# Kernel tuning notes

Measured on AMD Instinct MI355X. Metric: run time of the kernel, lower is better.

Reference implementation:

```python
import jax, jax.numpy as jnp
import numpy as np

N_NODES = 50000
N_EDGES = 800000
IN_FEAT = 256
OUT_FEAT = 256
NUM_RELS = 64
NUM_BASES = 8


def setup_inputs() -> dict:
    key = jax.random.key(0)
    ks = jax.random.split(key, 9)
    x = jax.random.normal(ks[0], (N_NODES, IN_FEAT), dtype=jnp.float32)
    src = jax.random.randint(ks[1], (N_EDGES,), 0, N_NODES, dtype=jnp.int32)
    dst = jax.random.randint(ks[2], (N_EDGES,), 0, N_NODES, dtype=jnp.int32)
    etypes = jax.random.randint(ks[3], (N_EDGES,), 0, NUM_RELS, dtype=jnp.int32)
    norm = jax.random.uniform(ks[4], (N_EDGES, 1), dtype=jnp.float32)
    # glorot-style params
    s_w = (6.0 / (IN_FEAT + OUT_FEAT)) ** 0.5
    weight = jax.random.uniform(ks[5], (NUM_BASES, IN_FEAT, OUT_FEAT), jnp.float32, -s_w, s_w)
    s_c = (6.0 / (NUM_RELS + NUM_BASES)) ** 0.5
    w_comp = jax.random.uniform(ks[6], (NUM_RELS, NUM_BASES), jnp.float32, -s_c, s_c)
    h_bias = jnp.zeros((OUT_FEAT,), jnp.float32)
    loop_weight = jax.random.uniform(ks[7], (IN_FEAT, OUT_FEAT), jnp.float32, -s_w, s_w)
    return {"x": x, "src": src, "dst": dst, "etypes": etypes, "norm": norm,
            "weight": weight, "w_comp": w_comp, "h_bias": h_bias,
            "loop_weight": loop_weight}


def reference(x, src, dst, etypes, norm, weight, w_comp, h_bias, loop_weight):
    # Basis regularizer with num_bases < num_rels:
    #   W_r = sum_b w_comp[r, b] * V_b
    # Per-edge message: msg_e = (x[src_e] @ W_{etype_e}) * norm_e,
    # aggregated by sum onto destination nodes. Since the map is linear,
    # we aggregate per basis first, then apply V_b (8 dense GEMMs).
    n_nodes = x.shape[0]
    coef = w_comp[etypes]                      # [E, B] per-edge basis coeffs
    xs = x[src] * norm                         # [E, D] normalized source feats
    out = jnp.zeros((n_nodes, weight.shape[2]), x.dtype)
    for b in range(weight.shape[0]):           # small fixed loop over bases
        agg = jax.ops.segment_sum(xs * coef[:, b:b + 1], dst,
                                  num_segments=n_nodes)   # [N, D]
        out = out + agg @ weight[b]            # [N, O]
    out = out + h_bias + x @ loop_weight       # bias + self-loop
    return jax.nn.relu(out)
```

## Files before the change

### kernel.cpp

```cpp
#include <hip/hip_runtime.h>
#include <hip/hip_bf16.h>
#include <stdint.h>

#define N_NODES 50000
#define N_EDGES 800000
#define IN_FEAT 256
#define OUT_FEAT 256
#define NUM_RELS 64
#define NUM_BASES 8
#define KTOT 2304
#define KAGG 2048
#define MP 50048
#define SCAN_BLKS 196

typedef __attribute__((ext_vector_type(8))) __bf16 bf16x8;
typedef __attribute__((ext_vector_type(4))) __bf16 bf16x4;
typedef __attribute__((ext_vector_type(4))) float f32x4;
typedef __attribute__((ext_vector_type(2))) float f32x2;

static __device__ __forceinline__ void gload_lds16(const void* g, void* l) {
  auto gp = (const __attribute__((address_space(1))) void*)(uintptr_t)g;
  auto lp = (__attribute__((address_space(3))) void*)(uint32_t)(uintptr_t)l;
  __builtin_amdgcn_global_load_lds(gp, lp, 16, 0, 0);
}

__global__ void k_prex(const float* __restrict__ x, __bf16* __restrict__ xb) {
  int i = blockIdx.x * 256 + threadIdx.x;
  const float4* xp = (const float4*)x;
  float4 u = xp[i * 2], v = xp[i * 2 + 1];
  bf16x8 o;
  o[0] = (__bf16)u.x; o[1] = (__bf16)u.y; o[2] = (__bf16)u.z; o[3] = (__bf16)u.w;
  o[4] = (__bf16)v.x; o[5] = (__bf16)v.y; o[6] = (__bf16)v.z; o[7] = (__bf16)v.w;
  *(bf16x8*)(xb + (size_t)i * 8) = o;
}

__global__ void k_count(const int* __restrict__ dst, int* __restrict__ deg) {
  int e = blockIdx.x * 256 + threadIdx.x;
  atomicAdd(&deg[dst[e]], 1);
}

__global__ void k_scan1(const int* __restrict__ deg, int* __restrict__ offs,
                        int* __restrict__ bsum) {
  __shared__ int s[256];
  int t = threadIdx.x;
  int i = blockIdx.x * 256 + t;
  int v = (i < N_NODES) ? deg[i] : 0;
  s[t] = v;
  __syncthreads();
  for (int d = 1; d < 256; d <<= 1) {
    int y = (t >= d) ? s[t - d] : 0;
    __syncthreads();
    s[t] += y;
    __syncthreads();
  }
  if (i < N_NODES) offs[i] = s[t] - v;
  if (t == 255) bsum[blockIdx.x] = s[255];
}

__global__ void k_scan3(int* __restrict__ offs, const int* __restrict__ bsum,
                        int* __restrict__ fill) {
  __shared__ int s[256];
  int t = threadIdx.x;
  s[t] = (t < SCAN_BLKS && t < blockIdx.x) ? bsum[t] : 0;
  __syncthreads();
  for (int d = 128; d; d >>= 1) {
    if (t < d) s[t] += s[t + d];
    __syncthreads();
  }
  int base = s[0];
  int i = blockIdx.x * 256 + t;
  if (i < N_NODES) {
    int o = offs[i] + base;
    offs[i] = o;
    fill[i] = o;
  }
}

__global__ void k_scatter(const int* __restrict__ dst, const int* __restrict__ srcv,
                          const int* __restrict__ ety, const float* __restrict__ norm,
                          int* __restrict__ fill, uint2* __restrict__ erec) {
  int e = blockIdx.x * 256 + threadIdx.x;
  int pos = atomicAdd(&fill[dst[e]], 1);
  erec[pos] = make_uint2((unsigned)srcv[e] | ((unsigned)ety[e] << 16),
                         __float_as_uint(norm[e]));
}

__global__ __launch_bounds__(256) void k_agg(
    const __bf16* __restrict__ xb, const float* __restrict__ w_comp,
    const int* __restrict__ offs, const int* __restrict__ fin,
    const uint2* __restrict__ erec, __bf16* __restrict__ A) {
  __shared__ float wc[NUM_RELS * NUM_BASES];
  int t = threadIdx.x;
  wc[t] = w_comp[t];
  wc[t + 256] = w_comp[t + 256];
  __syncthreads();

  int wid = t >> 6, lane = t & 63;
  int node = blockIdx.x * 4 + wid;

  f32x2 acc[NUM_BASES][2];
#pragma unroll
  for (int b = 0; b < NUM_BASES; ++b) {
    acc[b][0] = f32x2{0.f, 0.f};
    acc[b][1] = f32x2{0.f, 0.f};
  }

  int i0 = offs[node];
  int cnt = fin[node] - i0;
  const uint2* rp = erec + i0;
  int lo4 = lane * 4;

  int i = 0;
  for (; i + 4 <= cnt; i += 4) {
    uint2 r[4];
#pragma unroll
    for (int j = 0; j < 4; ++j) r[j] = rp[i + j];
    uint2 xv[4];
#pragma unroll
    for (int j = 0; j < 4; ++j)
      xv[j] = *(const uint2*)(xb + (size_t)(r[j].x & 0xffff) * IN_FEAT + lo4);
#pragma unroll
    for (int j = 0; j < 4; ++j) {
      int et = r[j].x >> 16;
      float nm = __uint_as_float(r[j].y);
      f32x2 v0 = {__uint_as_float(xv[j].x << 16) * nm,
                  __uint_as_float(xv[j].x & 0xffff0000u) * nm};
      f32x2 v1 = {__uint_as_float(xv[j].y << 16) * nm,
                  __uint_as_float(xv[j].y & 0xffff0000u) * nm};
      f32x4 cl = *(const f32x4*)&wc[et * 8];
      f32x4 ch = *(const f32x4*)&wc[et * 8 + 4];
#pragma unroll
      for (int b = 0; b < 4; ++b) {
        acc[b][0] += v0 * cl[b];
        acc[b][1] += v1 * cl[b];
        acc[b + 4][0] += v0 * ch[b];
        acc[b + 4][1] += v1 * ch[b];
      }
    }
  }
  for (; i < cnt; ++i) {
    uint2 r = rp[i];
    int et = r.x >> 16;
    float nm = __uint_as_float(r.y);
    uint2 xv = *(const uint2*)(xb + (size_t)(r.x & 0xffff) * IN_FEAT + lo4);
    f32x2 v0 = {__uint_as_float(xv.x << 16) * nm,
                __uint_as_float(xv.x & 0xffff0000u) * nm};
    f32x2 v1 = {__uint_as_float(xv.y << 16) * nm,
                __uint_as_float(xv.y & 0xffff0000u) * nm};
    f32x4 cl = *(const f32x4*)&wc[et * 8];
    f32x4 ch = *(const f32x4*)&wc[et * 8 + 4];
#pragma unroll
    for (int b = 0; b < 4; ++b) {
      acc[b][0] += v0 * cl[b];
      acc[b][1] += v1 * cl[b];
      acc[b + 4][0] += v0 * ch[b];
      acc[b + 4][1] += v1 * ch[b];
    }
  }

  __bf16* Ar = A + (size_t)node * KAGG + lo4;
#pragma unroll
  for (int b = 0; b < NUM_BASES; ++b) {
    bf16x4 o;
    o[0] = (__bf16)acc[b][0][0];
    o[1] = (__bf16)acc[b][0][1];
    o[2] = (__bf16)acc[b][1][0];
    o[3] = (__bf16)acc[b][1][1];
    *(bf16x4*)(Ar + b * 256) = o;
  }
}

__global__ void k_prepw(const float* __restrict__ weight, const float* __restrict__ loop_w,
                        __bf16* __restrict__ Wt) {
  int o = blockIdx.x;
  int t = threadIdx.x;
#pragma unroll
  for (int c = 0; c < 9; ++c) {
    int r = c * 256 + t;
    float v = (r < 2048) ? weight[(size_t)r * 256 + o]
                         : loop_w[(size_t)(r - 2048) * 256 + o];
    Wt[(size_t)o * KTOT + r] = (__bf16)v;
  }
}

__global__ __launch_bounds__(256, 2) void k_gemm(const __bf16* __restrict__ A,
                                                 const __bf16* __restrict__ xb,
                                                 const __bf16* __restrict__ Wt,
                                                 const float* __restrict__ bias,
                                                 float* __restrict__ out) {
  __shared__ __align__(16) __bf16 sA[3 * 128 * 32];
  __shared__ __align__(16) __bf16 sB[3 * 256 * 32];

  int t = threadIdx.x;
  int wid = t >> 6, lane = t & 63;
  int tm = blockIdx.x;
  int wr = wid >> 1, wc = wid & 1;
  int rfw = __builtin_amdgcn_readfirstlane(wid);

  f32x4 acc[4][8];
#pragma unroll
  for (int m = 0; m < 4; ++m)
#pragma unroll
    for (int n = 0; n < 8; ++n) acc[m][n] = f32x4{0.f, 0.f, 0.f, 0.f};

  int frow = lane & 15;
  int kb = (((lane >> 4) ^ ((frow >> 1) & 3)) << 4);

  const __bf16* gaP[2];
  const __bf16* gxP[2];
#pragma unroll
  for (int it = 0; it < 2; ++it) {
    int L = it * 256 + t;
    int row = L >> 2;
    int q = (L & 3) ^ ((row >> 1) & 3);
    gaP[it] = A + (size_t)(tm * 128 + row) * KAGG + q * 8;
    gxP[it] = xb + (size_t)(tm * 128 + row) * IN_FEAT + q * 8;
  }
  const __bf16* gbP[4];
#pragma unroll
  for (int it = 0; it < 4; ++it) {
    int L = it * 256 + t;
    int row = L >> 2;
    int q = (L & 3) ^ ((row >> 1) & 3);
    gbP[it] = Wt + (size_t)row * KTOT + q * 8;
  }

#define VMWAIT(N) asm volatile("s_waitcnt vmcnt(" #N ")" ::: "memory")
#define BARRIER()                                   \
  do {                                              \
    asm volatile("" ::: "memory");                  \
    __builtin_amdgcn_s_barrier();                   \
    asm volatile("" ::: "memory");                  \
  } while (0)

#define STAGE(KT, BUF)                                                        \
  do {                                                                        \
    int k0_ = (KT) * 32;                                                      \
    const __bf16 *a0_, *a1_;                                                  \
    if ((KT) < 64) { a0_ = gaP[0] + k0_; a1_ = gaP[1] + k0_; }                \
    else { int kx_ = k0_ - KAGG; a0_ = gxP[0] + kx_; a1_ = gxP[1] + kx_; }    \
    char* bA_ = (char*)sA + (BUF) * 8192;                                     \
    char* bB_ = (char*)sB + (BUF) * 16384;                                    \
    gload_lds16(a0_, bA_ + rfw * 1024);                                       \
    gload_lds16(a1_, bA_ + 4096 + rfw * 1024);                                \
    _Pragma("unroll") for (int it = 0; it < 4; ++it)                          \
        gload_lds16(gbP[it] + k0_, bB_ + (it * 256 + rfw * 64) * 16);         \
  } while (0)

#define COMPUTE(BUF)                                                          \
  do {                                                                        \
    const char* bA_ = (const char*)sA + (BUF) * 8192;                         \
    const char* bB_ = (const char*)sB + (BUF) * 16384;                        \
    bf16x8 af[4], bfr[8];                                                     \
    _Pragma("unroll") for (int m = 0; m < 4; ++m)                             \
        af[m] = *(const bf16x8*)(bA_ + (wr * 64 + m * 16 + frow) * 64 + kb);  \
    _Pragma("unroll") for (int n = 0; n < 8; ++n)                             \
        bfr[n] = *(const bf16x8*)(bB_ + (wc * 128 + n * 16 + frow) * 64 + kb);\
    _Pragma("unroll") for (int m = 0; m < 4; ++m)                             \
        _Pragma("unroll") for (int n = 0; n < 8; ++n)                         \
            acc[m][n] = __builtin_amdgcn_mfma_f32_16x16x32_bf16(              \
                af[m], bfr[n], acc[m][n], 0, 0, 0);                           \
  } while (0)

  STAGE(0, 0);
  STAGE(1, 1);
  STAGE(2, 2);

#define STEP(KT, BUF)                                                         \
  do {                                                                        \
    VMWAIT(12);           \
    BARRIER();                       \
    COMPUTE(BUF);                                                             \
    BARRIER();               \
    STAGE((KT) + 3, BUF);                                                     \
  } while (0)

  for (int k3 = 0; k3 < 69; k3 += 3) {
    STEP(k3 + 0, 0);
    STEP(k3 + 1, 1);
    STEP(k3 + 2, 2);
  }
  VMWAIT(12); BARRIER(); COMPUTE(0);
  VMWAIT(6);  BARRIER(); COMPUTE(1);
  VMWAIT(0);  BARRIER(); COMPUTE(2);
#undef STEP
#undef STAGE
#undef COMPUTE
#undef VMWAIT
#undef BARRIER

  int r0 = (lane >> 4) * 4;
  int c0 = lane & 15;
#pragma unroll
  for (int m = 0; m < 4; ++m) {
    int rowb = tm * 128 + wr * 64 + m * 16 + r0;
#pragma unroll
    for (int n = 0; n < 8; ++n) {
      int col = wc * 128 + n * 16 + c0;
      float bv = bias[col];
#pragma unroll
      for (int r = 0; r < 4; ++r) {
        int row = rowb + r;
        if (row < N_NODES) {
          float v = acc[m][n][r] + bv;
          out[(size_t)row * OUT_FEAT + col] = v > 0.f ? v : 0.f;
        }
      }
    }
  }
}

extern "C" void kernel_launch(void* const* d_in, const int* in_sizes, int n_in,
                              void* d_out, int out_size, void* d_ws, size_t ws_size,
                              hipStream_t stream) {
  const float* x      = (const float*)d_in[0];
  const int*   src    = (const int*)d_in[1];
  const int*   dst    = (const int*)d_in[2];
  const int*   ety    = (const int*)d_in[3];
  const float* norm   = (const float*)d_in[4];
  const float* weight = (const float*)d_in[5];
  const float* w_comp = (const float*)d_in[6];
  const float* h_bias = (const float*)d_in[7];
  const float* loop_w = (const float*)d_in[8];
  float* out = (float*)d_out;

  char* ws = (char*)d_ws;
  __bf16* A  = (__bf16*)ws;
  size_t off = (size_t)MP * KAGG * 2;
  __bf16* xb = (__bf16*)(ws + off);
  off += (size_t)MP * IN_FEAT * 2;
  __bf16* Wt = (__bf16*)(ws + off);
  off += (size_t)256 * KTOT * 2;
  uint2* erec = (uint2*)(ws + off);
  off += (size_t)N_EDGES * 8;
  int* deg   = (int*)(ws + off);
  int* offs  = deg + N_NODES;
  int* fill  = offs + N_NODES;
  int* bsum  = fill + N_NODES;

  hipMemsetAsync(deg, 0, N_NODES * sizeof(int), stream);
  k_prex<<<(N_NODES * IN_FEAT / 8) / 256, 256, 0, stream>>>(x, xb);
  k_count<<<N_EDGES / 256, 256, 0, stream>>>(dst, deg);
  k_scan1<<<SCAN_BLKS, 256, 0, stream>>>(deg, offs, bsum);
  k_scan3<<<SCAN_BLKS, 256, 0, stream>>>(offs, bsum, fill);
  k_scatter<<<N_EDGES / 256, 256, 0, stream>>>(dst, src, ety, norm, fill, erec);
  k_agg<<<N_NODES / 4, 256, 0, stream>>>(xb, w_comp, offs, fill, erec, A);
  k_prepw<<<256, 256, 0, stream>>>(weight, loop_w, Wt);
  k_gemm<<<MP / 128, 256, 0, stream>>>(A, xb, Wt, h_bias, out);
}
```

Before: 319.1 us.

## Double GEMM K-tile to 64 and unroll edge aggregation by eight

The GEMM K-step grows from 32 to 64, which doubles the LDS buffers and changes the swizzle to an 8-chunk XOR layout. The step count drops from 72 to 36 and occupancy falls to one block per SIMD via launch bounds. This halves the barrier and wait overhead per MFMA but raises LDS use and may reduce latency hiding. The aggregation kernel also gains an 8-way unrolled edge loop so more gathers are in flight, at the cost of extra registers.

```diff
diff --git a/kernel.cpp b/kernel.cpp
--- a/kernel.cpp
+++ b/kernel.cpp
@@ -85,6 +85,24 @@
                          __float_as_uint(norm[e]));
 }
 
+#define AGG_BODY(RX, RY, XV)                                                  \
+  do {                                                                        \
+    int et_ = (RX) >> 16;                                                     \
+    float nm_ = __uint_as_float(RY);                                          \
+    f32x2 v0_ = {__uint_as_float((XV).x << 16) * nm_,                         \
+                 __uint_as_float((XV).x & 0xffff0000u) * nm_};                 \
+    f32x2 v1_ = {__uint_as_float((XV).y << 16) * nm_,                         \
+                 __uint_as_float((XV).y & 0xffff0000u) * nm_};                 \
+    f32x4 cl_ = *(const f32x4*)&wc[et_ * 8];                                  \
+    f32x4 ch_ = *(const f32x4*)&wc[et_ * 8 + 4];                              \
+    _Pragma("unroll") for (int b = 0; b < 4; ++b) {                           \
+      acc[b][0] += v0_ * cl_[b];                                              \
+      acc[b][1] += v1_ * cl_[b];                                              \
+      acc[b + 4][0] += v0_ * ch_[b];                                          \
+      acc[b + 4][1] += v1_ * ch_[b];                                          \
+    }                                                                         \
+  } while (0)
+
 __global__ __launch_bounds__(256) void k_agg(
     const __bf16* __restrict__ xb, const float* __restrict__ w_comp,
     const int* __restrict__ offs, const int* __restrict__ fin,
@@ -111,6 +129,17 @@
   int lo4 = lane * 4;
 
   int i = 0;
+  for (; i + 8 <= cnt; i += 8) {
+    uint2 r[8];
+#pragma unroll
+    for (int j = 0; j < 8; ++j) r[j] = rp[i + j];
+    uint2 xv[8];
+#pragma unroll
+    for (int j = 0; j < 8; ++j)
+      xv[j] = *(const uint2*)(xb + (size_t)(r[j].x & 0xffff) * IN_FEAT + lo4);
+#pragma unroll
+    for (int j = 0; j < 8; ++j) AGG_BODY(r[j].x, r[j].y, xv[j]);
+  }
   for (; i + 4 <= cnt; i += 4) {
     uint2 r[4];
 #pragma unroll
@@ -120,42 +149,12 @@
     for (int j = 0; j < 4; ++j)
       xv[j] = *(const uint2*)(xb + (size_t)(r[j].x & 0xffff) * IN_FEAT + lo4);
 #pragma unroll
-    for (int j = 0; j < 4; ++j) {
-      int et = r[j].x >> 16;
-      float nm = __uint_as_float(r[j].y);
-      f32x2 v0 = {__uint_as_float(xv[j].x << 16) * nm,
-                  __uint_as_float(xv[j].x & 0xffff0000u) * nm};
-      f32x2 v1 = {__uint_as_float(xv[j].y << 16) * nm,
-                  __uint_as_float(xv[j].y & 0xffff0000u) * nm};
-      f32x4 cl = *(const f32x4*)&wc[et * 8];
-      f32x4 ch = *(const f32x4*)&wc[et * 8 + 4];
-#pragma unroll
-      for (int b = 0; b < 4; ++b) {
-        acc[b][0] += v0 * cl[b];
-        acc[b][1] += v1 * cl[b];
-        acc[b + 4][0] += v0 * ch[b];
-        acc[b + 4][1] += v1 * ch[b];
-      }
-    }
+    for (int j = 0; j < 4; ++j) AGG_BODY(r[j].x, r[j].y, xv[j]);
   }
   for (; i < cnt; ++i) {
     uint2 r = rp[i];
-    int et = r.x >> 16;
-    float nm = __uint_as_float(r.y);
     uint2 xv = *(const uint2*)(xb + (size_t)(r.x & 0xffff) * IN_FEAT + lo4);
-    f32x2 v0 = {__uint_as_float(xv.x << 16) * nm,
-                __uint_as_float(xv.x & 0xffff0000u) * nm};
-    f32x2 v1 = {__uint_as_float(xv.y << 16) * nm,
-                __uint_as_float(xv.y & 0xffff0000u) * nm};
-    f32x4 cl = *(const f32x4*)&wc[et * 8];
-    f32x4 ch = *(const f32x4*)&wc[et * 8 + 4];
-#pragma unroll
-    for (int b = 0; b < 4; ++b) {
-      acc[b][0] += v0 * cl[b];
-      acc[b][1] += v1 * cl[b];
-      acc[b + 4][0] += v0 * ch[b];
-      acc[b + 4][1] += v1 * ch[b];
-    }
+    AGG_BODY(r.x, r.y, xv);
   }
 
   __bf16* Ar = A + (size_t)node * KAGG + lo4;
@@ -183,13 +182,13 @@
   }
 }
 
-__global__ __launch_bounds__(256, 2) void k_gemm(const __bf16* __restrict__ A,
+__global__ __launch_bounds__(256, 1) void k_gemm(const __bf16* __restrict__ A,
                                                  const __bf16* __restrict__ xb,
                                                  const __bf16* __restrict__ Wt,
                                                  const float* __restrict__ bias,
                                                  float* __restrict__ out) {
-  __shared__ __align__(16) __bf16 sA[3 * 128 * 32];
-  __shared__ __align__(16) __bf16 sB[3 * 256 * 32];
+  __shared__ __align__(16) __bf16 sA[3 * 128 * 64];
+  __shared__ __align__(16) __bf16 sB[3 * 256 * 64];
 
   int t = threadIdx.x;
   int wid = t >> 6, lane = t & 63;
@@ -204,25 +203,25 @@
     for (int n = 0; n < 8; ++n) acc[m][n] = f32x4{0.f, 0.f, 0.f, 0.f};
 
   int frow = lane & 15;
-  int kb = (((lane >> 4) ^ ((frow >> 1) & 3)) << 4);
-
-  const __bf16* gaP[2];
-  const __bf16* gxP[2];
-#pragma unroll
-  for (int it = 0; it < 2; ++it) {
-    int L = it * 256 + t;
-    int row = L >> 2;
-    int q = (L & 3) ^ ((row >> 1) & 3);
-    gaP[it] = A + (size_t)(tm * 128 + row) * KAGG + q * 8;
-    gxP[it] = xb + (size_t)(tm * 128 + row) * IN_FEAT + q * 8;
-  }
-  const __bf16* gbP[4];
+  int g = lane >> 4;
+  int f7 = lane & 7;
+  int kb0 = ((g ^ f7) << 4);
+  int kb1 = (((4 + g) ^ f7) << 4);
+
+  int qoff = ((t & 7) ^ ((t >> 3) & 7)) * 8;
+  const __bf16* gaP[4];
+  const __bf16* gxP[4];
 #pragma unroll
   for (int it = 0; it < 4; ++it) {
-    int L = it * 256 + t;
-    int row = L >> 2;
-    int q = (L & 3) ^ ((row >> 1) & 3);
-    gbP[it] = Wt + (size_t)row * KTOT + q * 8;
+    int row = it * 32 + (t >> 3);
+    gaP[it] = A + (size_t)(tm * 128 + row) * KAGG + qoff;
+    gxP[it] = xb + (size_t)(tm * 128 + row) * IN_FEAT + qoff;
+  }
+  const __bf16* gbP[8];
+#pragma unroll
+  for (int it = 0; it < 8; ++it) {
+    int row = it * 32 + (t >> 3);
+    gbP[it] = Wt + (size_t)row * KTOT + qoff;
   }
 
 #define VMWAIT(N) asm volatile("s_waitcnt vmcnt(" #N ")" ::: "memory")
@@ -235,31 +234,47 @@
 
 #define STAGE(KT, BUF)                                                        \
   do {                                                                        \
-    int k0_ = (KT) * 32;                                                      \
-    const __bf16 *a0_, *a1_;                                                  \
-    if ((KT) < 64) { a0_ = gaP[0] + k0_; a1_ = gaP[1] + k0_; }                \
-    else { int kx_ = k0_ - KAGG; a0_ = gxP[0] + kx_; a1_ = gxP[1] + kx_; }    \
-    char* bA_ = (char*)sA + (BUF) * 8192;                                     \
-    char* bB_ = (char*)sB + (BUF) * 16384;                                    \
-    gload_lds16(a0_, bA_ + rfw * 1024);                                       \
-    gload_lds16(a1_, bA_ + 4096 + rfw * 1024);                                \
-    _Pragma("unroll") for (int it = 0; it < 4; ++it)                          \
+    int k0_ = (KT) * 64;                                                      \
+    char* bA_ = (char*)sA + (BUF) * 16384;                                    \
+    char* bB_ = (char*)sB + (BUF) * 32768;                                    \
+    if ((KT) < 32) {                                                          \
+      _Pragma("unroll") for (int it = 0; it < 4; ++it)                        \
+          gload_lds16(gaP[it] + k0_, bA_ + (it * 256 + rfw * 64) * 16);       \
+    } else {                                                                  \
+      int kx_ = k0_ - KAGG;                                                   \
+      _Pragma("unroll") for (int it = 0; it < 4; ++it)                        \
+          gload_lds16(gxP[it] + kx_, bA_ + (it * 256 + rfw * 64) * 16);       \
+    }                                                                         \
+    _Pragma("unroll") for (int it = 0; it < 8; ++it)                          \
         gload_lds16(gbP[it] + k0_, bB_ + (it * 256 + rfw * 64) * 16);         \
   } while (0)
 
 #define COMPUTE(BUF)                                                          \
   do {                                                                        \
-    const char* bA_ = (const char*)sA + (BUF) * 8192;                         \
-    const char* bB_ = (const char*)sB + (BUF) * 16384;                        \
-    bf16x8 af[4], bfr[8];                                                     \
-    _Pragma("unroll") for (int m = 0; m < 4; ++m)                             \
-        af[m] = *(const bf16x8*)(bA_ + (wr * 64 + m * 16 + frow) * 64 + kb);  \
-    _Pragma("unroll") for (int n = 0; n < 8; ++n)                             \
-        bfr[n] = *(const bf16x8*)(bB_ + (wc * 128 + n * 16 + frow) * 64 + kb);\
-    _Pragma("unroll") for (int m = 0; m < 4; ++m)                             \
-        _Pragma("unroll") for (int n = 0; n < 8; ++n)                         \
-            acc[m][n] = __builtin_amdgcn_mfma_f32_16x16x32_bf16(              \
-                af[m], bfr[n], acc[m][n], 0, 0, 0);                           \
+    const char* bA_ = (const char*)sA + (BUF) * 16384;                        \
+    const char* bB_ = (const char*)sB + (BUF) * 32768;                        \
+    {                                                                         \
+      bf16x8 af[4], bfr[8];                                                   \
+      _Pragma("unroll") for (int m = 0; m < 4; ++m)                           \
+          af[m] = *(const bf16x8*)(bA_ + (wr * 64 + m * 16 + frow) * 128 + kb0);\
+      _Pragma("unroll") for (int n = 0; n < 8; ++n)                           \
+          bfr[n] = *(const bf16x8*)(bB_ + (wc * 128 + n * 16 + frow) * 128 + kb0);\
+      _Pragma("unroll") for (int m = 0; m < 4; ++m)                           \
+          _Pragma("unroll") for (int n = 0; n < 8; ++n)                       \
+              acc[m][n] = __builtin_amdgcn_mfma_f32_16x16x32_bf16(            \
+                  af[m], bfr[n], acc[m][n], 0, 0, 0);                         \
+    }                                                                         \
+    {                                                                         \
+      bf16x8 af[4], bfr[8];                                                   \
+      _Pragma("unroll") for (int m = 0; m < 4; ++m)                           \
+          af[m] = *(const bf16x8*)(bA_ + (wr * 64 + m * 16 + frow) * 128 + kb1);\
+      _Pragma("unroll") for (int n = 0; n < 8; ++n)                           \
+          bfr[n] = *(const bf16x8*)(bB_ + (wc * 128 + n * 16 + frow) * 128 + kb1);\
+      _Pragma("unroll") for (int m = 0; m < 4; ++m)                           \
+          _Pragma("unroll") for (int n = 0; n < 8; ++n)                       \
+              acc[m][n] = __builtin_amdgcn_mfma_f32_16x16x32_bf16(            \
+                  af[m], bfr[n], acc[m][n], 0, 0, 0);                         \
+    }                                                                         \
   } while (0)
 
   STAGE(0, 0);
@@ -268,20 +283,20 @@
 
 #define STEP(KT, BUF)                                                         \
   do {                                                                        \
-    VMWAIT(12);           \
+    VMWAIT(24);          \
     BARRIER();                       \
     COMPUTE(BUF);                                                             \
     BARRIER();               \
     STAGE((KT) + 3, BUF);                                                     \
   } while (0)
 
-  for (int k3 = 0; k3 < 69; k3 += 3) {
+  for (int k3 = 0; k3 < 33; k3 += 3) {
     STEP(k3 + 0, 0);
     STEP(k3 + 1, 1);
     STEP(k3 + 2, 2);
   }
-  VMWAIT(12); BARRIER(); COMPUTE(0);
-  VMWAIT(6);  BARRIER(); COMPUTE(1);
+  VMWAIT(24); BARRIER(); COMPUTE(0);
+  VMWAIT(12); BARRIER(); COMPUTE(1);
   VMWAIT(0);  BARRIER(); COMPUTE(2);
 #undef STEP
 #undef STAGE
```

Result: slower. 328.7 us (+3.0%).
